# Kernel optimization log

Hardware: AMD Instinct MI355X
Metric: run time of the kernel (lower is better)

## Reference

```python
import jax, jax.numpy as jnp
import numpy as np

NUM_USERS = 100000
NUM_ITEMS = 50000
N_NODES = NUM_USERS + NUM_ITEMS
EMBED_DIM = 64
NUM_LAYERS = 3
NUM_EDGES = 1250000
EDGE_ATTR_DIM = 7
MLP_HID = 32
AUDIO_SCALE = 1.0
META_SCALE = 0.5


def _l2norm(x, eps=1e-12):
    # F.normalize(p=2, dim=-1): x / max(||x||, eps)
    n = jnp.sqrt(jnp.sum(x * x, axis=-1, keepdims=True))
    return x / jnp.maximum(n, eps)


def setup_inputs() -> dict:
    key = jax.random.key(0)
    ks = jax.random.split(key, 12)
    return {
        'user_emb_w': jax.random.normal(ks[0], (NUM_USERS, EMBED_DIM), jnp.float32),
        'artist_emb_w': jax.random.normal(ks[1], (20000, EMBED_DIM), jnp.float32),
        'album_emb_w': jax.random.normal(ks[2], (40000, EMBED_DIM), jnp.float32),
        'item_audio': jax.random.normal(ks[3], (NUM_ITEMS, EMBED_DIM), jnp.float32),
        'edge_attr': jax.random.normal(ks[4], (NUM_EDGES, EDGE_ATTR_DIM), jnp.float32),
        'edge_weight_init': jax.random.uniform(ks[5], (NUM_EDGES,), jnp.float32),
        'w1': jax.random.normal(ks[6], (EDGE_ATTR_DIM + 1, MLP_HID), jnp.float32),
        'b1': jnp.zeros((MLP_HID,), jnp.float32),
        'w2': jax.random.normal(ks[7], (MLP_HID, 1), jnp.float32),
        'b2': jnp.zeros((1,), jnp.float32),
        'edge_index': jax.random.randint(ks[8], (2, NUM_EDGES), 0, N_NODES, jnp.int64 if jax.config.read('jax_enable_x64') else jnp.int32),
        'artist_ids': jax.random.randint(ks[9], (NUM_ITEMS,), 0, 20000, jnp.int32),
        'album_ids': jax.random.randint(ks[10], (NUM_ITEMS,), 0, 40000, jnp.int32),
    }


def reference(user_emb_w, artist_emb_w, album_emb_w, item_audio, edge_attr,
              edge_weight_init, w1, b1, w2, b2, edge_index, artist_ids, album_ids):
    # Edge weight MLP: Linear -> ReLU -> Linear -> Sigmoid, squeezed
    ef = jnp.concatenate([edge_attr, edge_weight_init[:, None]], axis=1)  # [E, 8]
    h = jax.nn.relu(ef @ w1 + b1)
    w = jax.nn.sigmoid(h @ w2 + b2)[:, 0]  # [E]

    # Node features
    user_embed = _l2norm(user_emb_w)                                   # [U, D]
    meta = (artist_emb_w[artist_ids] + album_emb_w[album_ids]) * META_SCALE
    item_embed = _l2norm(item_audio * AUDIO_SCALE + meta)              # [I, D]
    x = jnp.concatenate([user_embed, item_embed], axis=0)              # [N, D]

    # gcn_norm (LGConv default, no self-loops): deg from target (col) scatter of w
    row, col = edge_index[0], edge_index[1]
    deg = jax.ops.segment_sum(w, col, num_segments=N_NODES)
    dinv = jnp.where(deg > 0, jax.lax.rsqrt(jnp.maximum(deg, 1e-30)), 0.0)
    norm = dinv[row] * w * dinv[col]                                   # [E]

    acc = x
    for _ in range(NUM_LAYERS):
        msg = norm[:, None] * x[row]                                   # [E, D]
        x = jax.ops.segment_sum(msg, col, num_segments=N_NODES)       # [N, D]
        acc = acc + x
    x = _l2norm(acc / (NUM_LAYERS + 1))

    user_emb = x[:NUM_USERS]
    item_emb = x[NUM_USERS:]
    align_loss = jnp.float32(0.0)
    return user_emb, item_emb, align_loss
```

## Files before the change

kernel.cpp:

```cpp
#include <hip/hip_runtime.h>
#include <hip/hip_bf16.h>
#include <math.h>

#define NUM_USERS  100000
#define NUM_ITEMS  50000
#define N_NODES    150000
#define EMBED_DIM  64
#define NUM_EDGES  1250000
#define MLP_HID    32
#define SCAN_B     1024
#define SCAN_NB    ((N_NODES + SCAN_B - 1) / SCAN_B)
#define NPW        4
#define PAD(x)     (((x) + 15) & ~15)

__global__ void hist_rank(const int* __restrict__ edge_index,
                          int* __restrict__ cnt,
                          int* __restrict__ rank) {
    int e = blockIdx.x * blockDim.x + threadIdx.x;
    if (e >= NUM_EDGES) return;
    int c = edge_index[NUM_EDGES + e];
    rank[e] = atomicAdd(&cnt[c], 1);
}

__global__ void scan_partial(const int* __restrict__ cnt,
                             int* __restrict__ part) {
    __shared__ int s[SCAN_B];
    int tid = threadIdx.x;
    int i = blockIdx.x * SCAN_B + tid;
    s[tid] = (i < N_NODES) ? PAD(cnt[i]) : 0;
    __syncthreads();
#pragma unroll
    for (int off = SCAN_B / 2; off > 0; off >>= 1) {
        if (tid < off) s[tid] += s[tid + off];
        __syncthreads();
    }
    if (tid == 0) part[blockIdx.x] = s[0];
}

__global__ void scan_offsets(const int* __restrict__ part,
                             int* __restrict__ base_off) {
    __shared__ int s[256];
    int tid = threadIdx.x;
    int v = (tid < SCAN_NB) ? part[tid] : 0;
    s[tid] = v;
    __syncthreads();
#pragma unroll
    for (int off = 1; off < 256; off <<= 1) {
        int t = (tid >= off) ? s[tid - off] : 0;
        __syncthreads();
        s[tid] += t;
        __syncthreads();
    }
    if (tid < SCAN_NB) base_off[tid] = s[tid] - v;
}

__global__ void scan_apply(const int* __restrict__ cnt,
                           const int* __restrict__ base_off,
                           int* __restrict__ row_ptr) {
    __shared__ int s[SCAN_B];
    int tid = threadIdx.x;
    int i = blockIdx.x * SCAN_B + tid;
    int v = (i < N_NODES) ? PAD(cnt[i]) : 0;
    s[tid] = v;
    __syncthreads();
    for (int off = 1; off < SCAN_B; off <<= 1) {
        int t = (tid >= off) ? s[tid - off] : 0;
        __syncthreads();
        s[tid] += t;
        __syncthreads();
    }
    if (i < N_NODES) row_ptr[i] = s[tid] - v + base_off[blockIdx.x];
    if (i == N_NODES - 1) row_ptr[N_NODES] = s[tid] + base_off[blockIdx.x];
}

__global__ void zero_pad(const int* __restrict__ cnt,
                         const int* __restrict__ row_ptr,
                         int2* __restrict__ csr_pair) {
    int t = blockIdx.x * blockDim.x + threadIdx.x;
    int node = t >> 4;
    int lane = t & 15;
    if (node >= N_NODES) return;
    int s = row_ptr[node] + cnt[node];
    int e = row_ptr[node + 1];
    int2 z; z.x = 0; z.y = 0;
    for (int j = s + lane; j < e; j += 16) csr_pair[j] = z;
}

__global__ void mlp_scatter(const float* __restrict__ edge_attr,
                            const float* __restrict__ ew,
                            const float* __restrict__ w1,
                            const float* __restrict__ b1,
                            const float* __restrict__ w2,
                            const float* __restrict__ b2,
                            const int*   __restrict__ edge_index,
                            const int*   __restrict__ rank,
                            const int*   __restrict__ row_ptr,
                            int2* __restrict__ csr_pair) {
    __shared__ float w1s[8 * MLP_HID];
    __shared__ float b1s[MLP_HID];
    __shared__ float w2s[MLP_HID];
    int tid = threadIdx.x;
    if (tid < 8 * MLP_HID) w1s[tid] = w1[tid];
    if (tid < MLP_HID) { b1s[tid] = b1[tid]; w2s[tid] = w2[tid]; }
    __syncthreads();

    int e = blockIdx.x * blockDim.x + tid;
    if (e >= NUM_EDGES) return;

    float ef[8];
#pragma unroll
    for (int k = 0; k < 7; ++k) ef[k] = edge_attr[e * 7 + k];
    ef[7] = ew[e];

    float s = b2[0];
#pragma unroll
    for (int j = 0; j < MLP_HID; ++j) {
        float h = b1s[j];
#pragma unroll
        for (int k = 0; k < 8; ++k) h = fmaf(ef[k], w1s[k * MLP_HID + j], h);
        h = fmaxf(h, 0.0f);
        s = fmaf(h, w2s[j], s);
    }
    float w = 1.0f / (1.0f + expf(-s));

    int r = edge_index[e];
    int c = edge_index[NUM_EDGES + e];
    int pos = row_ptr[c] + rank[e];
    int2 pr;
    pr.x = r;
    pr.y = __float_as_int(w);
    csr_pair[pos] = pr;
}

__global__ void deg_dinv_csr(const int* __restrict__ row_ptr,
                             const int* __restrict__ cnt,
                             const int2* __restrict__ csr_pair,
                             float* __restrict__ dinv) {
    int t = blockIdx.x * blockDim.x + threadIdx.x;
    int node = t >> 4;
    int lane = t & 15;
    if (node >= N_NODES) return;
    int s = row_ptr[node], e = s + cnt[node];
    float sum = 0.0f;
    for (int j = s + lane; j < e; j += 16) sum += __int_as_float(csr_pair[j].y);
    sum += __shfl_xor(sum, 8);
    sum += __shfl_xor(sum, 4);
    sum += __shfl_xor(sum, 2);
    sum += __shfl_xor(sum, 1);
    if (lane == 0)
        dinv[node] = (sum > 0.0f) ? rsqrtf(fmaxf(sum, 1e-30f)) : 0.0f;
}

__global__ void csr_scale(const int* __restrict__ row_ptr,
                          const int* __restrict__ cnt,
                          const float* __restrict__ dinv,
                          int2* __restrict__ csr_pair) {
    int t = blockIdx.x * blockDim.x + threadIdx.x;
    int node = t >> 4;
    int lane = t & 15;
    if (node >= N_NODES) return;
    int s = row_ptr[node], e = s + cnt[node];
    float dc = dinv[node];
    for (int j = s + lane; j < e; j += 16) {
        int2 p = csr_pair[j];
        p.y = __float_as_int(__int_as_float(p.y) * dc * dinv[p.x]);
        csr_pair[j] = p;
    }
}

__global__ void init_x(const float* __restrict__ user_w,
                       const float* __restrict__ artist_w,
                       const float* __restrict__ album_w,
                       const float* __restrict__ audio,
                       const int*   __restrict__ artist_ids,
                       const int*   __restrict__ album_ids,
                       __hip_bfloat16* __restrict__ x) {
    int t = blockIdx.x * blockDim.x + threadIdx.x;
    int row = t >> 6;
    int lane = t & 63;
    if (row >= N_NODES) return;

    float v;
    if (row < NUM_USERS) {
        v = user_w[row * EMBED_DIM + lane];
    } else {
        int r = row - NUM_USERS;
        int ar = artist_ids[r];
        int al = album_ids[r];
        v = audio[r * EMBED_DIM + lane]
          + 0.5f * (artist_w[ar * EMBED_DIM + lane] + album_w[al * EMBED_DIM + lane]);
    }
    float ss = v * v;
#pragma unroll
    for (int off = 32; off > 0; off >>= 1) ss += __shfl_xor(ss, off);
    float scale = 1.0f / fmaxf(sqrtf(ss), 1e-12f);
    x[row * EMBED_DIM + lane] = __float2bfloat16(v * scale);
}

#define BF_LO(u) __uint_as_float((u) << 16)
#define BF_HI(u) __uint_as_float((u) & 0xffff0000u)

__global__ void propagate_mid(const int* __restrict__ row_ptr,
                              const int2* __restrict__ csr_pair,
                              const unsigned short* __restrict__ xin,
                              unsigned short* __restrict__ xout) {
    int wave = (blockIdx.x * blockDim.x + threadIdx.x) >> 6;
    int lane = threadIdx.x & 63;
    int node0 = wave * NPW;
    if (node0 >= N_NODES) return;

    int eg = lane >> 4;
    int dq = (lane & 15) << 2;

    int rpv = row_ptr[node0 + (lane <= NPW ? lane : NPW)];
    int rs0 = __shfl(rpv, 0);
    int rs1 = __shfl(rpv, 1);
    int rs2 = __shfl(rpv, 2);
    int rs3 = __shfl(rpv, 3);
    int rs4 = __shfl(rpv, 4);

    int j = rs0 + (eg << 2);
    int2 p0 = csr_pair[j];
    int2 p1 = csr_pair[j + 1];
    int2 p2 = csr_pair[j + 2];
    int2 p3 = csr_pair[j + 3];

#pragma unroll
    for (int k = 0; k < NPW; ++k) {
        int bs = (k == 0) ? rs0 : (k == 1) ? rs1 : (k == 2) ? rs2 : rs3;
        int be = (k == 0) ? rs1 : (k == 1) ? rs2 : (k == 2) ? rs3 : rs4;
        float a0 = 0, a1 = 0, a2 = 0, a3 = 0;

        for (int base = bs; base < be; base += 16) {
            int   s0 = p0.x; float w0 = __int_as_float(p0.y);
            int   s1 = p1.x; float w1 = __int_as_float(p1.y);
            int   s2 = p2.x; float w2 = __int_as_float(p2.y);
            int   s3 = p3.x; float w3 = __int_as_float(p3.y);

            uint2 u0 = *(const uint2*)(xin + ((size_t)s0 << 6) + dq);
            uint2 u1 = *(const uint2*)(xin + ((size_t)s1 << 6) + dq);
            uint2 u2 = *(const uint2*)(xin + ((size_t)s2 << 6) + dq);
            uint2 u3 = *(const uint2*)(xin + ((size_t)s3 << 6) + dq);

            j += 16;
            p0 = csr_pair[j];
            p1 = csr_pair[j + 1];
            p2 = csr_pair[j + 2];
            p3 = csr_pair[j + 3];

            a0 = fmaf(w0, BF_LO(u0.x), a0); a1 = fmaf(w0, BF_HI(u0.x), a1);
            a2 = fmaf(w0, BF_LO(u0.y), a2); a3 = fmaf(w0, BF_HI(u0.y), a3);
            a0 = fmaf(w1, BF_LO(u1.x), a0); a1 = fmaf(w1, BF_HI(u1.x), a1);
            a2 = fmaf(w1, BF_LO(u1.y), a2); a3 = fmaf(w1, BF_HI(u1.y), a3);
            a0 = fmaf(w2, BF_LO(u2.x), a0); a1 = fmaf(w2, BF_HI(u2.x), a1);
            a2 = fmaf(w2, BF_LO(u2.y), a2); a3 = fmaf(w2, BF_HI(u2.y), a3);
            a0 = fmaf(w3, BF_LO(u3.x), a0); a1 = fmaf(w3, BF_HI(u3.x), a1);
            a2 = fmaf(w3, BF_LO(u3.y), a2); a3 = fmaf(w3, BF_HI(u3.y), a3);
        }

        a0 += __shfl_xor(a0, 16); a1 += __shfl_xor(a1, 16);
        a2 += __shfl_xor(a2, 16); a3 += __shfl_xor(a3, 16);
        a0 += __shfl_xor(a0, 32); a1 += __shfl_xor(a1, 32);
        a2 += __shfl_xor(a2, 32); a3 += __shfl_xor(a3, 32);

        if (eg == 0) {
            size_t o = ((size_t)(node0 + k) << 6) + dq;
            unsigned int b0 = (unsigned int)__bfloat16_as_ushort(__float2bfloat16(a0));
            unsigned int b1 = (unsigned int)__bfloat16_as_ushort(__float2bfloat16(a1));
            unsigned int b2 = (unsigned int)__bfloat16_as_ushort(__float2bfloat16(a2));
            unsigned int b3 = (unsigned int)__bfloat16_as_ushort(__float2bfloat16(a3));
            uint2 u;
            u.x = b0 | (b1 << 16);
            u.y = b2 | (b3 << 16);
            *(uint2*)(xout + o) = u;
        }
    }
}

__global__ void propagate_final(const int* __restrict__ row_ptr,
                                const int2* __restrict__ csr_pair,
                                const unsigned short* __restrict__ x0,
                                const unsigned short* __restrict__ x1,
                                const unsigned short* __restrict__ x2,
                                float* __restrict__ outp) {
    int wave = (blockIdx.x * blockDim.x + threadIdx.x) >> 6;
    int lane = threadIdx.x & 63;
    int node0 = wave * NPW;
    if (node0 >= N_NODES) return;

    int eg = lane >> 4;
    int dq = (lane & 15) << 2;

    int rpv = row_ptr[node0 + (lane <= NPW ? lane : NPW)];
    int rs0 = __shfl(rpv, 0);
    int rs1 = __shfl(rpv, 1);
    int rs2 = __shfl(rpv, 2);
    int rs3 = __shfl(rpv, 3);
    int rs4 = __shfl(rpv, 4);

    int j = rs0 + (eg << 2);
    int2 p0 = csr_pair[j];
    int2 p1 = csr_pair[j + 1];
    int2 p2 = csr_pair[j + 2];
    int2 p3 = csr_pair[j + 3];

#pragma unroll
    for (int k = 0; k < NPW; ++k) {
        int bs = (k == 0) ? rs0 : (k == 1) ? rs1 : (k == 2) ? rs2 : rs3;
        int be = (k == 0) ? rs1 : (k == 1) ? rs2 : (k == 2) ? rs3 : rs4;
        float a0 = 0, a1 = 0, a2 = 0, a3 = 0;

        for (int base = bs; base < be; base += 16) {
            int   s0 = p0.x; float w0 = __int_as_float(p0.y);
            int   s1 = p1.x; float w1 = __int_as_float(p1.y);
            int   s2 = p2.x; float w2 = __int_as_float(p2.y);
            int   s3 = p3.x; float w3 = __int_as_float(p3.y);

            uint2 u0 = *(const uint2*)(x2 + ((size_t)s0 << 6) + dq);
            uint2 u1 = *(const uint2*)(x2 + ((size_t)s1 << 6) + dq);
            uint2 u2 = *(const uint2*)(x2 + ((size_t)s2 << 6) + dq);
            uint2 u3 = *(const uint2*)(x2 + ((size_t)s3 << 6) + dq);

            j += 16;
            p0 = csr_pair[j];
            p1 = csr_pair[j + 1];
            p2 = csr_pair[j + 2];
            p3 = csr_pair[j + 3];

            a0 = fmaf(w0, BF_LO(u0.x), a0); a1 = fmaf(w0, BF_HI(u0.x), a1);
            a2 = fmaf(w0, BF_LO(u0.y), a2); a3 = fmaf(w0, BF_HI(u0.y), a3);
            a0 = fmaf(w1, BF_LO(u1.x), a0); a1 = fmaf(w1, BF_HI(u1.x), a1);
            a2 = fmaf(w1, BF_LO(u1.y), a2); a3 = fmaf(w1, BF_HI(u1.y), a3);
            a0 = fmaf(w2, BF_LO(u2.x), a0); a1 = fmaf(w2, BF_HI(u2.x), a1);
            a2 = fmaf(w2, BF_LO(u2.y), a2); a3 = fmaf(w2, BF_HI(u2.y), a3);
            a0 = fmaf(w3, BF_LO(u3.x), a0); a1 = fmaf(w3, BF_HI(u3.x), a1);
            a2 = fmaf(w3, BF_LO(u3.y), a2); a3 = fmaf(w3, BF_HI(u3.y), a3);
        }

        a0 += __shfl_xor(a0, 16); a1 += __shfl_xor(a1, 16);
        a2 += __shfl_xor(a2, 16); a3 += __shfl_xor(a3, 16);
        a0 += __shfl_xor(a0, 32); a1 += __shfl_xor(a1, 32);
        a2 += __shfl_xor(a2, 32); a3 += __shfl_xor(a3, 32);

        if (eg == 0) {
            size_t o = ((size_t)(node0 + k) << 6) + dq;
            uint2 u0 = *(const uint2*)(x0 + o);
            uint2 u1 = *(const uint2*)(x1 + o);
            uint2 u2 = *(const uint2*)(x2 + o);

            float v0 = (BF_LO(u0.x) + BF_LO(u1.x) + BF_LO(u2.x) + a0) * 0.25f;
            float v1 = (BF_HI(u0.x) + BF_HI(u1.x) + BF_HI(u2.x) + a1) * 0.25f;
            float v2 = (BF_LO(u0.y) + BF_LO(u1.y) + BF_LO(u2.y) + a2) * 0.25f;
            float v3 = (BF_HI(u0.y) + BF_HI(u1.y) + BF_HI(u2.y) + a3) * 0.25f;

            float ss = v0 * v0 + v1 * v1 + v2 * v2 + v3 * v3;
            ss += __shfl_xor(ss, 1);
            ss += __shfl_xor(ss, 2);
            ss += __shfl_xor(ss, 4);
            ss += __shfl_xor(ss, 8);
            float scale = 1.0f / fmaxf(sqrtf(ss), 1e-12f);

            float4 r = { v0 * scale, v1 * scale, v2 * scale, v3 * scale };
            *(float4*)(outp + o) = r;
        }
    }
    if (blockIdx.x == 0 && threadIdx.x == 0)
        outp[(size_t)N_NODES * EMBED_DIM] = 0.0f;
}

#undef BF_LO
#undef BF_HI

extern "C" void kernel_launch(void* const* d_in, const int* in_sizes, int n_in,
                              void* d_out, int out_size, void* d_ws, size_t ws_size,
                              hipStream_t stream) {
    const float* user_w     = (const float*)d_in[0];
    const float* artist_w   = (const float*)d_in[1];
    const float* album_w    = (const float*)d_in[2];
    const float* audio      = (const float*)d_in[3];
    const float* edge_attr  = (const float*)d_in[4];
    const float* ew         = (const float*)d_in[5];
    const float* w1         = (const float*)d_in[6];
    const float* b1         = (const float*)d_in[7];
    const float* w2         = (const float*)d_in[8];
    const float* b2         = (const float*)d_in[9];
    const int*   edge_index = (const int*)d_in[10];
    const int*   artist_ids = (const int*)d_in[11];
    const int*   album_ids  = (const int*)d_in[12];
    float* out = (float*)d_out;

    float* ws = (float*)d_ws;
    unsigned short* x0 = (unsigned short*)ws;
    unsigned short* x1 = (unsigned short*)(ws + 4800000);
    unsigned short* x2 = (unsigned short*)(ws + 9600000);
    int*  row_ptr  = (int*)(ws + 14400000);
    int2* csr_pair = (int2*)(ws + 14560000);
    int*   cnt     = (int*)ws;
    int*   rank    = (int*)(ws + 150000);
    int*   part    = (int*)(ws + 1400000);
    int*   baseoff = (int*)(ws + 1401000);
    float* dinv    = ws + 1402000;

    const int B = 256;
    const int egrid   = (NUM_EDGES + B - 1) / B;
    const int ngrid   = (N_NODES * EMBED_DIM) / B;
    const int ngrid16 = (N_NODES * 16) / B;
    const int pgrid   = (N_NODES / NPW * 64) / B;

    hipMemsetAsync(cnt, 0, N_NODES * sizeof(int), stream);

    hist_rank<<<egrid, B, 0, stream>>>(edge_index, cnt, rank);

    scan_partial<<<SCAN_NB, SCAN_B, 0, stream>>>(cnt, part);
    scan_offsets<<<1, 256, 0, stream>>>(part, baseoff);
    scan_apply<<<SCAN_NB, SCAN_B, 0, stream>>>(cnt, baseoff, row_ptr);

    zero_pad<<<ngrid16, B, 0, stream>>>(cnt, row_ptr, csr_pair);

    mlp_scatter<<<egrid, B, 0, stream>>>(
        edge_attr, ew, w1, b1, w2, b2, edge_index, rank, row_ptr, csr_pair);

    deg_dinv_csr<<<ngrid16, B, 0, stream>>>(row_ptr, cnt, csr_pair, dinv);
    csr_scale<<<ngrid16, B, 0, stream>>>(row_ptr, cnt, dinv, csr_pair);

    init_x<<<ngrid, B, 0, stream>>>(
        user_w, artist_w, album_w, audio, artist_ids, album_ids,
        (__hip_bfloat16*)x0);

    propagate_mid<<<pgrid, B, 0, stream>>>(row_ptr, csr_pair, x0, x1);
    propagate_mid<<<pgrid, B, 0, stream>>>(row_ptr, csr_pair, x1, x2);
    propagate_final<<<pgrid, B, 0, stream>>>(row_ptr, csr_pair, x0, x1, x2, out);
}
```

Baseline: 421.0 us.

## Fuse MLP into histogram, build CSR via permutation, apply dinv in propagation

Computes the edge MLP in the histogram pass and writes edge-ordered (row, weight) pairs. A small perm scatter followed by a gather-based CSR build replaces the random 8-byte scatter, and it also computes degrees. Zero padding is merged into the same pass and the padding granularity drops from 16 to 8. The csr_scale pass is removed by applying the source dinv gather and destination dinv scaling inside each propagation kernel. The cost is an extra random dinv load per edge in every layer, plus a narrower 2-edge-per-lane inner loop in propagation.

Result: faster. 401.2 us (-4.7%).

```diff
diff --git a/kernel.cpp b/kernel.cpp
--- a/kernel.cpp
+++ b/kernel.cpp
@@ -11,15 +11,52 @@
 #define SCAN_B     1024
 #define SCAN_NB    ((N_NODES + SCAN_B - 1) / SCAN_B)
 #define NPW        4
-#define PAD(x)     (((x) + 15) & ~15)
-
-__global__ void hist_rank(const int* __restrict__ edge_index,
-                          int* __restrict__ cnt,
-                          int* __restrict__ rank) {
-    int e = blockIdx.x * blockDim.x + threadIdx.x;
+#define PAD(x)     (((x) + 7) & ~7)
+
+__global__ void hist_mlp(const float* __restrict__ edge_attr,
+                         const float* __restrict__ ew,
+                         const float* __restrict__ w1,
+                         const float* __restrict__ b1,
+                         const float* __restrict__ w2,
+                         const float* __restrict__ b2,
+                         const int*   __restrict__ edge_index,
+                         int*  __restrict__ cnt,
+                         int*  __restrict__ rank,
+                         int2* __restrict__ epair) {
+    __shared__ float w1s[8 * MLP_HID];
+    __shared__ float b1s[MLP_HID];
+    __shared__ float w2s[MLP_HID];
+    int tid = threadIdx.x;
+    if (tid < 8 * MLP_HID) w1s[tid] = w1[tid];
+    if (tid < MLP_HID) { b1s[tid] = b1[tid]; w2s[tid] = w2[tid]; }
+    __syncthreads();
+
+    int e = blockIdx.x * blockDim.x + tid;
     if (e >= NUM_EDGES) return;
+
     int c = edge_index[NUM_EDGES + e];
     rank[e] = atomicAdd(&cnt[c], 1);
+
+    float ef[8];
+#pragma unroll
+    for (int k = 0; k < 7; ++k) ef[k] = edge_attr[e * 7 + k];
+    ef[7] = ew[e];
+
+    float s = b2[0];
+#pragma unroll
+    for (int j = 0; j < MLP_HID; ++j) {
+        float h = b1s[j];
+#pragma unroll
+        for (int k = 0; k < 8; ++k) h = fmaf(ef[k], w1s[k * MLP_HID + j], h);
+        h = fmaxf(h, 0.0f);
+        s = fmaf(h, w2s[j], s);
+    }
+    float w = 1.0f / (1.0f + expf(-s));
+
+    int2 pr;
+    pr.x = edge_index[e];
+    pr.y = __float_as_int(w);
+    epair[e] = pr;
 }
 
 __global__ void scan_partial(const int* __restrict__ cnt,
@@ -73,99 +110,47 @@
     if (i == N_NODES - 1) row_ptr[N_NODES] = s[tid] + base_off[blockIdx.x];
 }
 
-__global__ void zero_pad(const int* __restrict__ cnt,
-                         const int* __restrict__ row_ptr,
-                         int2* __restrict__ csr_pair) {
+__global__ void scatter_perm(const int* __restrict__ edge_index,
+                             const int* __restrict__ rank,
+                             const int* __restrict__ row_ptr,
+                             int* __restrict__ perm) {
+    int e = blockIdx.x * blockDim.x + threadIdx.x;
+    if (e >= NUM_EDGES) return;
+    int c = edge_index[NUM_EDGES + e];
+    perm[row_ptr[c] + rank[e]] = e;
+}
+
+__global__ void pair_build(const int* __restrict__ row_ptr,
+                           const int* __restrict__ cnt,
+                           const int* __restrict__ perm,
+                           const int2* __restrict__ epair,
+                           int2* __restrict__ csr_pair,
+                           float* __restrict__ dinv) {
     int t = blockIdx.x * blockDim.x + threadIdx.x;
     int node = t >> 4;
     int lane = t & 15;
     if (node >= N_NODES) return;
-    int s = row_ptr[node] + cnt[node];
+    int s = row_ptr[node];
     int e = row_ptr[node + 1];
-    int2 z; z.x = 0; z.y = 0;
-    for (int j = s + lane; j < e; j += 16) csr_pair[j] = z;
-}
-
-__global__ void mlp_scatter(const float* __restrict__ edge_attr,
-                            const float* __restrict__ ew,
-                            const float* __restrict__ w1,
-                            const float* __restrict__ b1,
-                            const float* __restrict__ w2,
-                            const float* __restrict__ b2,
-                            const int*   __restrict__ edge_index,
-                            const int*   __restrict__ rank,
-                            const int*   __restrict__ row_ptr,
-                            int2* __restrict__ csr_pair) {
-    __shared__ float w1s[8 * MLP_HID];
-    __shared__ float b1s[MLP_HID];
-    __shared__ float w2s[MLP_HID];
-    int tid = threadIdx.x;
-    if (tid < 8 * MLP_HID) w1s[tid] = w1[tid];
-    if (tid < MLP_HID) { b1s[tid] = b1[tid]; w2s[tid] = w2[tid]; }
-    __syncthreads();
-
-    int e = blockIdx.x * blockDim.x + tid;
-    if (e >= NUM_EDGES) return;
-
-    float ef[8];
-#pragma unroll
-    for (int k = 0; k < 7; ++k) ef[k] = edge_attr[e * 7 + k];
-    ef[7] = ew[e];
-
-    float s = b2[0];
-#pragma unroll
-    for (int j = 0; j < MLP_HID; ++j) {
-        float h = b1s[j];
-#pragma unroll
-        for (int k = 0; k < 8; ++k) h = fmaf(ef[k], w1s[k * MLP_HID + j], h);
-        h = fmaxf(h, 0.0f);
-        s = fmaf(h, w2s[j], s);
-    }
-    float w = 1.0f / (1.0f + expf(-s));
-
-    int r = edge_index[e];
-    int c = edge_index[NUM_EDGES + e];
-    int pos = row_ptr[c] + rank[e];
-    int2 pr;
-    pr.x = r;
-    pr.y = __float_as_int(w);
-    csr_pair[pos] = pr;
-}
-
-__global__ void deg_dinv_csr(const int* __restrict__ row_ptr,
-                             const int* __restrict__ cnt,
-                             const int2* __restrict__ csr_pair,
-                             float* __restrict__ dinv) {
-    int t = blockIdx.x * blockDim.x + threadIdx.x;
-    int node = t >> 4;
-    int lane = t & 15;
-    if (node >= N_NODES) return;
-    int s = row_ptr[node], e = s + cnt[node];
+    int re = s + cnt[node];
     float sum = 0.0f;
-    for (int j = s + lane; j < e; j += 16) sum += __int_as_float(csr_pair[j].y);
+    for (int j = s + lane; j < e; j += 16) {
+        int2 pr;
+        if (j < re) {
+            int eid = perm[j];
+            pr = epair[eid];
+            sum += __int_as_float(pr.y);
+        } else {
+            pr.x = 0; pr.y = 0;
+        }
+        csr_pair[j] = pr;
+    }
     sum += __shfl_xor(sum, 8);
     sum += __shfl_xor(sum, 4);
     sum += __shfl_xor(sum, 2);
     sum += __shfl_xor(sum, 1);
     if (lane == 0)
         dinv[node] = (sum > 0.0f) ? rsqrtf(fmaxf(sum, 1e-30f)) : 0.0f;
-}
-
-__global__ void csr_scale(const int* __restrict__ row_ptr,
-                          const int* __restrict__ cnt,
-                          const float* __restrict__ dinv,
-                          int2* __restrict__ csr_pair) {
-    int t = blockIdx.x * blockDim.x + threadIdx.x;
-    int node = t >> 4;
-    int lane = t & 15;
-    if (node >= N_NODES) return;
-    int s = row_ptr[node], e = s + cnt[node];
-    float dc = dinv[node];
-    for (int j = s + lane; j < e; j += 16) {
-        int2 p = csr_pair[j];
-        p.y = __float_as_int(__int_as_float(p.y) * dc * dinv[p.x]);
-        csr_pair[j] = p;
-    }
 }
 
 __global__ void init_x(const float* __restrict__ user_w,
@@ -202,6 +187,7 @@
 
 __global__ void propagate_mid(const int* __restrict__ row_ptr,
                               const int2* __restrict__ csr_pair,
+                              const float* __restrict__ dinv,
                               const unsigned short* __restrict__ xin,
                               unsigned short* __restrict__ xout) {
     int wave = (blockIdx.x * blockDim.x + threadIdx.x) >> 6;
@@ -219,11 +205,9 @@
     int rs3 = __shfl(rpv, 3);
     int rs4 = __shfl(rpv, 4);
 
-    int j = rs0 + (eg << 2);
-    int2 p0 = csr_pair[j];
-    int2 p1 = csr_pair[j + 1];
-    int2 p2 = csr_pair[j + 2];
-    int2 p3 = csr_pair[j + 3];
+    int j = rs0 + eg;
+    int2 pa = csr_pair[j];
+    int2 pb = csr_pair[j + 4];
 
 #pragma unroll
     for (int k = 0; k < NPW; ++k) {
@@ -231,31 +215,24 @@
         int be = (k == 0) ? rs1 : (k == 1) ? rs2 : (k == 2) ? rs3 : rs4;
         float a0 = 0, a1 = 0, a2 = 0, a3 = 0;
 
-        for (int base = bs; base < be; base += 16) {
-            int   s0 = p0.x; float w0 = __int_as_float(p0.y);
-            int   s1 = p1.x; float w1 = __int_as_float(p1.y);
-            int   s2 = p2.x; float w2 = __int_as_float(p2.y);
-            int   s3 = p3.x; float w3 = __int_as_float(p3.y);
-
-            uint2 u0 = *(const uint2*)(xin + ((size_t)s0 << 6) + dq);
-            uint2 u1 = *(const uint2*)(xin + ((size_t)s1 << 6) + dq);
-            uint2 u2 = *(const uint2*)(xin + ((size_t)s2 << 6) + dq);
-            uint2 u3 = *(const uint2*)(xin + ((size_t)s3 << 6) + dq);
-
-            j += 16;
-            p0 = csr_pair[j];
-            p1 = csr_pair[j + 1];
-            p2 = csr_pair[j + 2];
-            p3 = csr_pair[j + 3];
-
-            a0 = fmaf(w0, BF_LO(u0.x), a0); a1 = fmaf(w0, BF_HI(u0.x), a1);
-            a2 = fmaf(w0, BF_LO(u0.y), a2); a3 = fmaf(w0, BF_HI(u0.y), a3);
-            a0 = fmaf(w1, BF_LO(u1.x), a0); a1 = fmaf(w1, BF_HI(u1.x), a1);
-            a2 = fmaf(w1, BF_LO(u1.y), a2); a3 = fmaf(w1, BF_HI(u1.y), a3);
-            a0 = fmaf(w2, BF_LO(u2.x), a0); a1 = fmaf(w2, BF_HI(u2.x), a1);
-            a2 = fmaf(w2, BF_LO(u2.y), a2); a3 = fmaf(w2, BF_HI(u2.y), a3);
-            a0 = fmaf(w3, BF_LO(u3.x), a0); a1 = fmaf(w3, BF_HI(u3.x), a1);
-            a2 = fmaf(w3, BF_LO(u3.y), a2); a3 = fmaf(w3, BF_HI(u3.y), a3);
+        for (int base = bs; base < be; base += 8) {
+            int   sa = pa.x; float wa = __int_as_float(pa.y);
+            int   sb = pb.x; float wb = __int_as_float(pb.y);
+            float da = dinv[sa];
+            float db = dinv[sb];
+            uint2 ua = *(const uint2*)(xin + ((size_t)sa << 6) + dq);
+            uint2 ub = *(const uint2*)(xin + ((size_t)sb << 6) + dq);
+
+            j += 8;
+            pa = csr_pair[j];
+            pb = csr_pair[j + 4];
+
+            float fa = wa * da;
+            float fb = wb * db;
+            a0 = fmaf(fa, BF_LO(ua.x), a0); a1 = fmaf(fa, BF_HI(ua.x), a1);
+            a2 = fmaf(fa, BF_LO(ua.y), a2); a3 = fmaf(fa, BF_HI(ua.y), a3);
+            a0 = fmaf(fb, BF_LO(ub.x), a0); a1 = fmaf(fb, BF_HI(ub.x), a1);
+            a2 = fmaf(fb, BF_LO(ub.y), a2); a3 = fmaf(fb, BF_HI(ub.y), a3);
         }
 
         a0 += __shfl_xor(a0, 16); a1 += __shfl_xor(a1, 16);
@@ -264,11 +241,12 @@
         a2 += __shfl_xor(a2, 32); a3 += __shfl_xor(a3, 32);
 
         if (eg == 0) {
+            float dc = dinv[node0 + k];
             size_t o = ((size_t)(node0 + k) << 6) + dq;
-            unsigned int b0 = (unsigned int)__bfloat16_as_ushort(__float2bfloat16(a0));
-            unsigned int b1 = (unsigned int)__bfloat16_as_ushort(__float2bfloat16(a1));
-            unsigned int b2 = (unsigned int)__bfloat16_as_ushort(__float2bfloat16(a2));
-            unsigned int b3 = (unsigned int)__bfloat16_as_ushort(__float2bfloat16(a3));
+            unsigned int b0 = (unsigned int)__bfloat16_as_ushort(__float2bfloat16(a0 * dc));
+            unsigned int b1 = (unsigned int)__bfloat16_as_ushort(__float2bfloat16(a1 * dc));
+            unsigned int b2 = (unsigned int)__bfloat16_as_ushort(__float2bfloat16(a2 * dc));
+            unsigned int b3 = (unsigned int)__bfloat16_as_ushort(__float2bfloat16(a3 * dc));
             uint2 u;
             u.x = b0 | (b1 << 16);
             u.y = b2 | (b3 << 16);
@@ -279,6 +257,7 @@
 
 __global__ void propagate_final(const int* __restrict__ row_ptr,
                                 const int2* __restrict__ csr_pair,
+                                const float* __restrict__ dinv,
                                 const unsigned short* __restrict__ x0,
                                 const unsigned short* __restrict__ x1,
                                 const unsigned short* __restrict__ x2,
@@ -298,11 +277,9 @@
     int rs3 = __shfl(rpv, 3);
     int rs4 = __shfl(rpv, 4);
 
-    int j = rs0 + (eg << 2);
-    int2 p0 = csr_pair[j];
-    int2 p1 = csr_pair[j + 1];
-    int2 p2 = csr_pair[j + 2];
-    int2 p3 = csr_pair[j + 3];
+    int j = rs0 + eg;
+    int2 pa = csr_pair[j];
+    int2 pb = csr_pair[j + 4];
 
 #pragma unroll
     for (int k = 0; k < NPW; ++k) {
@@ -310,31 +287,24 @@
         int be = (k == 0) ? rs1 : (k == 1) ? rs2 : (k == 2) ? rs3 : rs4;
         float a0 = 0, a1 = 0, a2 = 0, a3 = 0;
 
-        for (int base = bs; base < be; base += 16) {
-            int   s0 = p0.x; float w0 = __int_as_float(p0.y);
-            int   s1 = p1.x; float w1 = __int_as_float(p1.y);
-            int   s2 = p2.x; float w2 = __int_as_float(p2.y);
-            int   s3 = p3.x; float w3 = __int_as_float(p3.y);
-
-            uint2 u0 = *(const uint2*)(x2 + ((size_t)s0 << 6) + dq);
-            uint2 u1 = *(const uint2*)(x2 + ((size_t)s1 << 6) + dq);
-            uint2 u2 = *(const uint2*)(x2 + ((size_t)s2 << 6) + dq);
-            uint2 u3 = *(const uint2*)(x2 + ((size_t)s3 << 6) + dq);
-
-            j += 16;
-            p0 = csr_pair[j];
-            p1 = csr_pair[j + 1];
-            p2 = csr_pair[j + 2];
-            p3 = csr_pair[j + 3];
-
-            a0 = fmaf(w0, BF_LO(u0.x), a0); a1 = fmaf(w0, BF_HI(u0.x), a1);
-            a2 = fmaf(w0, BF_LO(u0.y), a2); a3 = fmaf(w0, BF_HI(u0.y), a3);
-            a0 = fmaf(w1, BF_LO(u1.x), a0); a1 = fmaf(w1, BF_HI(u1.x), a1);
-            a2 = fmaf(w1, BF_LO(u1.y), a2); a3 = fmaf(w1, BF_HI(u1.y), a3);
-            a0 = fmaf(w2, BF_LO(u2.x), a0); a1 = fmaf(w2, BF_HI(u2.x), a1);
-            a2 = fmaf(w2, BF_LO(u2.y), a2); a3 = fmaf(w2, BF_HI(u2.y), a3);
-            a0 = fmaf(w3, BF_LO(u3.x), a0); a1 = fmaf(w3, BF_HI(u3.x), a1);
-            a2 = fmaf(w3, BF_LO(u3.y), a2); a3 = fmaf(w3, BF_HI(u3.y), a3);
+        for (int base = bs; base < be; base += 8) {
+            int   sa = pa.x; float wa = __int_as_float(pa.y);
+            int   sb = pb.x; float wb = __int_as_float(pb.y);
+            float da = dinv[sa];
+            float db = dinv[sb];
+            uint2 ua = *(const uint2*)(x2 + ((size_t)sa << 6) + dq);
+            uint2 ub = *(const uint2*)(x2 + ((size_t)sb << 6) + dq);
+
+            j += 8;
+            pa = csr_pair[j];
+            pb = csr_pair[j + 4];
+
+            float fa = wa * da;
+            float fb = wb * db;
+            a0 = fmaf(fa, BF_LO(ua.x), a0); a1 = fmaf(fa, BF_HI(ua.x), a1);
+            a2 = fmaf(fa, BF_LO(ua.y), a2); a3 = fmaf(fa, BF_HI(ua.y), a3);
+            a0 = fmaf(fb, BF_LO(ub.x), a0); a1 = fmaf(fb, BF_HI(ub.x), a1);
+            a2 = fmaf(fb, BF_LO(ub.y), a2); a3 = fmaf(fb, BF_HI(ub.y), a3);
         }
 
         a0 += __shfl_xor(a0, 16); a1 += __shfl_xor(a1, 16);
@@ -343,15 +313,16 @@
         a2 += __shfl_xor(a2, 32); a3 += __shfl_xor(a3, 32);
 
         if (eg == 0) {
+            float dc = dinv[node0 + k];
             size_t o = ((size_t)(node0 + k) << 6) + dq;
             uint2 u0 = *(const uint2*)(x0 + o);
             uint2 u1 = *(const uint2*)(x1 + o);
             uint2 u2 = *(const uint2*)(x2 + o);
 
-            float v0 = (BF_LO(u0.x) + BF_LO(u1.x) + BF_LO(u2.x) + a0) * 0.25f;
-            float v1 = (BF_HI(u0.x) + BF_HI(u1.x) + BF_HI(u2.x) + a1) * 0.25f;
-            float v2 = (BF_LO(u0.y) + BF_LO(u1.y) + BF_LO(u2.y) + a2) * 0.25f;
-            float v3 = (BF_HI(u0.y) + BF_HI(u1.y) + BF_HI(u2.y) + a3) * 0.25f;
+            float v0 = (BF_LO(u0.x) + BF_LO(u1.x) + BF_LO(u2.x) + a0 * dc) * 0.25f;
+            float v1 = (BF_HI(u0.x) + BF_HI(u1.x) + BF_HI(u2.x) + a1 * dc) * 0.25f;
+            float v2 = (BF_LO(u0.y) + BF_LO(u1.y) + BF_LO(u2.y) + a2 * dc) * 0.25f;
+            float v3 = (BF_HI(u0.y) + BF_HI(u1.y) + BF_HI(u2.y) + a3 * dc) * 0.25f;
 
             float ss = v0 * v0 + v1 * v1 + v2 * v2 + v3 * v3;
             ss += __shfl_xor(ss, 1);
@@ -393,13 +364,15 @@
     unsigned short* x0 = (unsigned short*)ws;
     unsigned short* x1 = (unsigned short*)(ws + 4800000);
     unsigned short* x2 = (unsigned short*)(ws + 9600000);
-    int*  row_ptr  = (int*)(ws + 14400000);
-    int2* csr_pair = (int2*)(ws + 14560000);
+    float* dinv    = ws + 14400000;
+    int*  row_ptr  = (int*)(ws + 14560000);
+    int2* csr_pair = (int2*)(ws + 14720000);
     int*   cnt     = (int*)ws;
     int*   rank    = (int*)(ws + 150000);
     int*   part    = (int*)(ws + 1400000);
     int*   baseoff = (int*)(ws + 1401000);
-    float* dinv    = ws + 1402000;
+    int2*  epair   = (int2*)(ws + 1500000);
+    int*   perm    = (int*)(ws + 4800000);
 
     const int B = 256;
     const int egrid   = (NUM_EDGES + B - 1) / B;
@@ -409,25 +382,23 @@
 
     hipMemsetAsync(cnt, 0, N_NODES * sizeof(int), stream);
 
-    hist_rank<<<egrid, B, 0, stream>>>(edge_index, cnt, rank);
+    hist_mlp<<<egrid, B, 0, stream>>>(
+        edge_attr, ew, w1, b1, w2, b2, edge_index, cnt, rank, epair);
 
     scan_partial<<<SCAN_NB, SCAN_B, 0, stream>>>(cnt, part);
     scan_offsets<<<1, 256, 0, stream>>>(part, baseoff);
     scan_apply<<<SCAN_NB, SCAN_B, 0, stream>>>(cnt, baseoff, row_ptr);
 
-    zero_pad<<<ngrid16, B, 0, stream>>>(cnt, row_ptr, csr_pair);
-
-    mlp_scatter<<<egrid, B, 0, stream>>>(
-        edge_attr, ew, w1, b1, w2, b2, edge_index, rank, row_ptr, csr_pair);
-
-    deg_dinv_csr<<<ngrid16, B, 0, stream>>>(row_ptr, cnt, csr_pair, dinv);
-    csr_scale<<<ngrid16, B, 0, stream>>>(row_ptr, cnt, dinv, csr_pair);
+    scatter_perm<<<egrid, B, 0, stream>>>(edge_index, rank, row_ptr, perm);
+
+    pair_build<<<ngrid16, B, 0, stream>>>(
+        row_ptr, cnt, perm, epair, csr_pair, dinv);
 
     init_x<<<ngrid, B, 0, stream>>>(
         user_w, artist_w, album_w, audio, artist_ids, album_ids,
         (__hip_bfloat16*)x0);
 
-    propagate_mid<<<pgrid, B, 0, stream>>>(row_ptr, csr_pair, x0, x1);
-    propagate_mid<<<pgrid, B, 0, stream>>>(row_ptr, csr_pair, x1, x2);
-    propagate_final<<<pgrid, B, 0, stream>>>(row_ptr, csr_pair, x0, x1, x2, out);
-}
+    propagate_mid<<<pgrid, B, 0, stream>>>(row_ptr, csr_pair, dinv, x0, x1);
+    propagate_mid<<<pgrid, B, 0, stream>>>(row_ptr, csr_pair, dinv, x1, x2);
+    propagate_final<<<pgrid, B, 0, stream>>>(row_ptr, csr_pair, dinv, x0, x1, x2, out);
+}
```
